# Kernel optimization log

Measured on AMD Instinct MI355X. Metric: run time of the kernel, lower is better.

## Reference

```python
import jax, jax.numpy as jnp
import numpy as np

N = 100000
E = 6400000
IN_CH = 128
HID = 8
HEADS = 2
OUT_CH = 1
NEG_SLOPE = 0.2


def gat_conv(x, src, dst, W, a_src, a_dst, bias, heads, out_ch, concat, n_nodes):
    # x: [N, F_in], W: [F_in, heads*out_ch], a_src/a_dst: [heads, out_ch]
    h = (x @ W).reshape(n_nodes, heads, out_ch)          # [N, H, C]
    alpha_s = jnp.sum(h * a_src[None], axis=-1)          # [N, H]
    alpha_d = jnp.sum(h * a_dst[None], axis=-1)          # [N, H]
    alpha = alpha_s[src] + alpha_d[dst]                  # [E, H]
    alpha = jax.nn.leaky_relu(alpha, NEG_SLOPE)
    # segment softmax over incoming edges of each destination node
    seg_max = jax.ops.segment_max(alpha, dst, num_segments=n_nodes)  # [N, H]
    alpha = jnp.exp(alpha - seg_max[dst])
    denom = jax.ops.segment_sum(alpha, dst, num_segments=n_nodes)    # [N, H]
    alpha = alpha / (denom[dst] + 1e-16)
    msg = h[src] * alpha[..., None]                       # [E, H, C]
    out = jax.ops.segment_sum(msg, dst, num_segments=n_nodes)        # [N, H, C]
    if concat:
        out = out.reshape(n_nodes, heads * out_ch)
    else:
        out = out.mean(axis=1)
    return out + bias


def setup_inputs() -> dict:
    key = jax.random.key(0)
    ks = jax.random.split(key, 12)
    x = jax.random.normal(ks[0], (N, IN_CH), dtype=jnp.float32)
    edge_index = jax.random.randint(ks[1], (2, E), 0, N, dtype=jnp.int64)
    s1 = 1.0 / np.sqrt(IN_CH)
    W1 = jax.random.normal(ks[2], (IN_CH, HEADS * HID), dtype=jnp.float32) * s1
    a_src1 = jax.random.normal(ks[3], (HEADS, HID), dtype=jnp.float32) * (1.0 / np.sqrt(HID))
    a_dst1 = jax.random.normal(ks[4], (HEADS, HID), dtype=jnp.float32) * (1.0 / np.sqrt(HID))
    b1 = jnp.zeros((HEADS * HID,), dtype=jnp.float32)
    s2 = 1.0 / np.sqrt(HEADS * HID)
    W2 = jax.random.normal(ks[5], (HEADS * HID, OUT_CH), dtype=jnp.float32) * s2
    a_src2 = jax.random.normal(ks[6], (1, OUT_CH), dtype=jnp.float32)
    a_dst2 = jax.random.normal(ks[7], (1, OUT_CH), dtype=jnp.float32)
    b2 = jnp.zeros((OUT_CH,), dtype=jnp.float32)
    return {"x": x, "edge_index": edge_index, "W1": W1, "a_src1": a_src1,
            "a_dst1": a_dst1, "b1": b1, "W2": W2, "a_src2": a_src2,
            "a_dst2": a_dst2, "b2": b2}


def reference(x, edge_index, W1, a_src1, a_dst1, b1, W2, a_src2, a_dst2, b2):
    # add self-loops (PyG GATConv default)
    loops = jnp.arange(N, dtype=edge_index.dtype)
    src = jnp.concatenate([edge_index[0], loops])
    dst = jnp.concatenate([edge_index[1], loops])
    h = gat_conv(x, src, dst, W1, a_src1, a_dst1, b1, HEADS, HID, True, N)
    h = jax.nn.relu(h)
    out = gat_conv(h, src, dst, W2, a_src2, a_dst2, b2, 1, OUT_CH, False, N)
    return out
```

## Files before the change

kernel.cpp:

```cpp
#include <hip/hip_runtime.h>
#include <hip/hip_fp16.h>
#include <cstdint>
#include <cstddef>

#define N_NODES 100000
#define E_EDGES 6400000
#define E_TOT   (E_EDGES + N_NODES)
#define IN_CH   128
#define NHID    16
#define BSHIFT  8
#define BSZ     256
#define NBUCK   391
#define CHUNK   8192
#define BCAP    24
#define NCHUNK  ((E_TOT + CHUNK - 1) / CHUNK)
#define LCAP    17664

__global__ void k_detect(const int* __restrict__ edge, int* __restrict__ flag) {
    if (blockIdx.x == 0 && threadIdx.x == 0) {
        int odd_or = 0;
        for (int i = 0; i < 64; i++) odd_or |= edge[2 * i + 1];
        flag[0] = (odd_or == 0) ? 1 : 0;
    }
}

__global__ __launch_bounds__(256) void k_gemm1(
        const float* __restrict__ x, const float* __restrict__ W1,
        const float* __restrict__ a_src1, const float* __restrict__ a_dst1,
        __half* __restrict__ h16, float* __restrict__ asrc,
        float* __restrict__ adst) {
    __shared__ __align__(16) float sW[IN_CH * NHID];
    __shared__ __align__(16) float sx[16][132];
    __shared__ float sh[16][17];
    int t = threadIdx.x;
    int r = t >> 4, c = t & 15;
    int row = blockIdx.x * 16 + r;

    const float4* W4 = (const float4*)W1;
    ((float4*)sW)[t] = W4[t];
    ((float4*)sW)[t + 256] = W4[t + 256];

    if (row < N_NODES) {
        const float4* xr = (const float4*)(x + (size_t)row * IN_CH);
        float4 v0 = xr[c];
        float4 v1 = xr[c + 16];
        *(float4*)&sx[r][4 * c] = v0;
        *(float4*)&sx[r][64 + 4 * c] = v1;
    }
    __syncthreads();

    float acc = 0.f;
    if (row < N_NODES) {
        #pragma unroll 16
        for (int k = 0; k < IN_CH; k++) acc = fmaf(sx[r][k], sW[k * NHID + c], acc);
        h16[(size_t)row * NHID + c] = __float2half(acc);
    }
    sh[r][c] = acc;
    __syncthreads();

    if (row < N_NODES && c < 4) {
        int h = c & 1;
        const float* av = (c >= 2) ? a_dst1 : a_src1;
        float s = 0.f;
        #pragma unroll
        for (int q = 0; q < 8; q++) s = fmaf(sh[r][h * 8 + q], av[h * 8 + q], s);
        if (c < 2) asrc[2 * (size_t)row + c] = s;
        else       adst[2 * (size_t)row + (c - 2)] = s;
    }
}

__global__ __launch_bounds__(256) void k_ccount(const int* __restrict__ edge,
                                                const int* __restrict__ flag,
                                                int* __restrict__ ccnt) {
    __shared__ int sc[NBUCK];
    int m64 = flag[0];
    int t = threadIdx.x;
    for (int i = t; i < NBUCK; i += 256) sc[i] = 0;
    __syncthreads();
    size_t c0 = (size_t)blockIdx.x * CHUNK;
    size_t cend = c0 + CHUNK; if (cend > E_TOT) cend = E_TOT;
    size_t ee = (cend < (size_t)E_EDGES) ? cend : (size_t)E_EDGES;

    if (m64) {
        const int4* dp = (const int4*)(edge + 2 * (size_t)E_EDGES);
        for (size_t i = c0 + 2 * t; i < ee; i += 512) {
            int4 v = dp[i >> 1];
            atomicAdd(&sc[v.x >> BSHIFT], 1);
            if (i + 1 < ee) atomicAdd(&sc[v.z >> BSHIFT], 1);
        }
    } else {
        const int4* dp = (const int4*)(edge + (size_t)E_EDGES);
        for (size_t i = c0 + 4 * t; i < ee; i += 1024) {
            int4 v = dp[i >> 2];
            atomicAdd(&sc[v.x >> BSHIFT], 1);
            if (i + 1 < ee) atomicAdd(&sc[v.y >> BSHIFT], 1);
            if (i + 2 < ee) atomicAdd(&sc[v.z >> BSHIFT], 1);
            if (i + 3 < ee) atomicAdd(&sc[v.w >> BSHIFT], 1);
        }
    }
    size_t sl0 = (c0 > (size_t)E_EDGES) ? c0 : (size_t)E_EDGES;
    for (size_t i = sl0 + t; i < cend; i += 256) {
        int d = (int)(i - E_EDGES);
        atomicAdd(&sc[d >> BSHIFT], 1);
    }
    __syncthreads();
    for (int i = t; i < NBUCK; i += 256)
        ccnt[(size_t)blockIdx.x * NBUCK + i] = sc[i];
}

__global__ __launch_bounds__(256) void k_cscan(int* __restrict__ ccnt,
                                               int* __restrict__ bcnt) {
    __shared__ int sd[256];
    __shared__ int carry;
    int b = blockIdx.x, t = threadIdx.x;
    if (t == 0) carry = 0;
    __syncthreads();
    for (int base = 0; base < NCHUNK; base += 256) {
        int c = base + t;
        int v = (c < NCHUNK) ? ccnt[(size_t)c * NBUCK + b] : 0;
        sd[t] = v;
        __syncthreads();
        for (int ofs = 1; ofs < 256; ofs <<= 1) {
            int a = sd[t];
            int bb = (t >= ofs) ? sd[t - ofs] : 0;
            __syncthreads();
            sd[t] = a + bb;
            __syncthreads();
        }
        if (c < NCHUNK) ccnt[(size_t)c * NBUCK + b] = sd[t] - v + carry;
        __syncthreads();
        if (t == 255) carry += sd[255];
        __syncthreads();
    }
    if (t == 0) bcnt[b] = carry;
}

__global__ __launch_bounds__(512) void k_bscan(const int* __restrict__ bcnt,
                                               int* __restrict__ bbase) {
    __shared__ int sd[512];
    int t = threadIdx.x;
    int v = (t < NBUCK) ? bcnt[t] : 0;
    sd[t] = v;
    __syncthreads();
    for (int ofs = 1; ofs < 512; ofs <<= 1) {
        int a = sd[t];
        int b = (t >= ofs) ? sd[t - ofs] : 0;
        __syncthreads();
        sd[t] = a + b;
        __syncthreads();
    }
    if (t < NBUCK) bbase[t] = sd[t] - v;
    if (t == NBUCK) bbase[NBUCK] = sd[NBUCK - 1];
}

__global__ __launch_bounds__(256) void k_bin(const int* __restrict__ edge,
                                             const int* __restrict__ flag,
                                             const int* __restrict__ ccnt,
                                             const int* __restrict__ bbase,
                                             unsigned* __restrict__ staged) {
    __shared__ unsigned lbin[NBUCK][BCAP];
    __shared__ int lcnt[NBUCK];
    __shared__ int lbase[NBUCK];
    int m64 = flag[0];
    int t = threadIdx.x;
    int g = t >> 4, lane = t & 15;

    size_t c0 = (size_t)blockIdx.x * CHUNK;
    if (c0 >= E_TOT) return;
    size_t cend = c0 + CHUNK; if (cend > E_TOT) cend = E_TOT;
    size_t ee = (cend < (size_t)E_EDGES) ? cend : (size_t)E_EDGES;

    for (int i = t; i < NBUCK; i += 256) {
        lcnt[i] = 0;
        lbase[i] = bbase[i] + ccnt[(size_t)blockIdx.x * NBUCK + i];
    }
    __syncthreads();

    auto put = [&](int s, int d) {
        int b = d >> BSHIFT;
        unsigned v = (unsigned)s | ((unsigned)(d & (BSZ - 1)) << 17);
        int idx = atomicAdd(&lcnt[b], 1);
        if (idx < BCAP) lbin[b][idx] = v;
        else            staged[lbase[b] + idx] = v;
    };

    if (m64) {
        const int4* sp = (const int4*)edge;
        const int4* dp = (const int4*)(edge + 2 * (size_t)E_EDGES);
        for (size_t i = c0 + 2 * t; i < ee; i += 512) {
            int4 sv = sp[i >> 1];
            int4 dv = dp[i >> 1];
            put(sv.x, dv.x);
            if (i + 1 < ee) put(sv.z, dv.z);
        }
    } else {
        const int4* sp = (const int4*)edge;
        const int4* dp = (const int4*)(edge + (size_t)E_EDGES);
        for (size_t i = c0 + 4 * t; i < ee; i += 1024) {
            int4 sv = sp[i >> 2];
            int4 dv = dp[i >> 2];
            put(sv.x, dv.x);
            if (i + 1 < ee) put(sv.y, dv.y);
            if (i + 2 < ee) put(sv.z, dv.z);
            if (i + 3 < ee) put(sv.w, dv.w);
        }
    }
    size_t sl0 = (c0 > (size_t)E_EDGES) ? c0 : (size_t)E_EDGES;
    for (size_t i = sl0 + t; i < cend; i += 256) {
        int d = (int)(i - E_EDGES);
        put(d, d);
    }
    __syncthreads();
    for (int b = g; b < NBUCK; b += 16) {
        int n = min(lcnt[b], BCAP);
        if (!n) continue;
        int pos = lbase[b];
        for (int i = lane; i < n; i += 16) staged[pos + i] = lbin[b][i];
    }
}

__global__ __launch_bounds__(512) void k_fused1(
        const unsigned* __restrict__ staged, const int* __restrict__ bbase,
        const __half* __restrict__ h16, const float* __restrict__ asrc,
        const float* __restrict__ adst,
        const float* __restrict__ b1, const float* __restrict__ W2,
        int* __restrict__ csr, int* __restrict__ offs,
        float* __restrict__ h2out) {
    __shared__ unsigned short lcsr16[LCAP];
    __shared__ unsigned hib[LCAP / 32];
    __shared__ int hist[BSZ];
    __shared__ int segbeg[BSZ];
    __shared__ int cur[BSZ];
    __shared__ float2 sadp[BSZ];
    int bkt = blockIdx.x;
    int t = threadIdx.x;
    int dbase = bkt << BSHIFT;
    int beg = bbase[bkt], end = bbase[bkt + 1];

    if (t < BSZ) {
        hist[t] = 0;
        int d = dbase + t;
        sadp[t] = (d < N_NODES) ? ((const float2*)adst)[d] : make_float2(0.f, 0.f);
    }
    for (int i = t; i < LCAP / 32; i += 512) hib[i] = 0;
    __syncthreads();
    for (int e = beg + t; e < end; e += 512)
        atomicAdd(&hist[staged[e] >> 17], 1);
    __syncthreads();

    int myv = (t < BSZ) ? hist[t] : 0;
    __syncthreads();
    for (int ofs = 1; ofs < BSZ; ofs <<= 1) {
        int a = 0, b = 0;
        if (t < BSZ) { a = hist[t]; b = (t >= ofs) ? hist[t - ofs] : 0; }
        __syncthreads();
        if (t < BSZ) hist[t] = a + b;
        __syncthreads();
    }
    if (t < BSZ) {
        int excl = hist[t] - myv;
        segbeg[t] = excl;
        cur[t] = excl;
        int d = dbase + t;
        if (d < N_NODES) offs[d] = beg + excl;
    }
    if (bkt == NBUCK - 1 && t == 0) offs[N_NODES] = E_TOT;
    __syncthreads();

    for (int e = beg + t; e < end; e += 512) {
        unsigned v = staged[e];
        int s = (int)(v & 0x1FFFFu);
        int pos = atomicAdd(&cur[v >> 17], 1);
        lcsr16[pos] = (unsigned short)s;
        if (s >> 16) atomicOr(&hib[pos >> 5], 1u << (pos & 31));
    }
    __syncthreads();

    auto getsrc = [&](int i) {
        return (int)lcsr16[i] | (int)(((hib[i >> 5] >> (i & 31)) & 1u) << 16);
    };

    int n = end - beg;
    for (int i = t; i < n; i += 512) csr[beg + i] = getsrc(i);

    int p = t >> 1, sub = t & 1;
    int sb = segbeg[p], se = cur[p];
    float adpv = sub ? sadp[p].y : sadp[p].x;

    float acc[8];
    #pragma unroll
    for (int c = 0; c < 8; c++) acc[c] = 0.f;
    float den = 0.f;

    auto loadslot = [&](int i, float& aspv, float4& hv) {
        if (i < se) {
            int s = getsrc(i);
            hv = *(const float4*)(h16 + (size_t)s * NHID + sub * 8);
            aspv = asrc[2 * (size_t)s + sub];
        }
    };
    auto consume = [&](float aspv, const float4& hv) {
        float a = aspv + adpv; a = (a > 0.f) ? a : 0.2f * a;
        float pw = __expf(a);
        den += pw;
        const __half2* hh = (const __half2*)&hv;
        #pragma unroll
        for (int q = 0; q < 4; q++) {
            float2 f = __half22float2(hh[q]);
            acc[2 * q]     = fmaf(pw, f.x, acc[2 * q]);
            acc[2 * q + 1] = fmaf(pw, f.y, acc[2 * q + 1]);
        }
    };

    float aA = 0.f, aB = 0.f, aC = 0.f, aD = 0.f, aE = 0.f, aF = 0.f;
    float4 z4 = make_float4(0.f, 0.f, 0.f, 0.f);
    float4 hA = z4, hB = z4, hC = z4, hD = z4, hE = z4, hF = z4;

    int i = sb;
    loadslot(i,     aA, hA);
    loadslot(i + 1, aB, hB);
    loadslot(i + 2, aC, hC);
    loadslot(i + 3, aD, hD);
    loadslot(i + 4, aE, hE);
    loadslot(i + 5, aF, hF);
    while (true) {
        if (i >= se) break;
        consume(aA, hA); loadslot(i + 6, aA, hA); i++;
        if (i >= se) break;
        consume(aB, hB); loadslot(i + 6, aB, hB); i++;
        if (i >= se) break;
        consume(aC, hC); loadslot(i + 6, aC, hC); i++;
        if (i >= se) break;
        consume(aD, hD); loadslot(i + 6, aD, hD); i++;
        if (i >= se) break;
        consume(aE, hE); loadslot(i + 6, aE, hE); i++;
        if (i >= se) break;
        consume(aF, hF); loadslot(i + 6, aF, hF); i++;
    }

    float inv = 1.f / (den + 1e-16f);
    float v = 0.f;
    #pragma unroll
    for (int ch = 0; ch < 8; ch++) {
        float o = acc[ch] * inv + b1[8 * sub + ch];
        o = (o > 0.f) ? o : 0.f;
        v = fmaf(o, W2[8 * sub + ch], v);
    }
    v += __shfl_xor(v, 1, 64);
    if (sub == 0) {
        int d = dbase + p;
        if (d < N_NODES) h2out[d] = v;
    }
}

__global__ __launch_bounds__(256) void k_edge2(
        const int* __restrict__ offs, const int* __restrict__ csr,
        const float* __restrict__ h2,
        const float* __restrict__ a_src2, const float* __restrict__ a_dst2,
        const float* __restrict__ b2, float* __restrict__ out) {
    int t = threadIdx.x;
    int g = t >> 4, lane = t & 15;
    int d = blockIdx.x * 16 + g;
    if (d >= N_NODES) return;

    float as2 = a_src2[0], ad2 = a_dst2[0];
    float adv = h2[d] * ad2;
    int beg = offs[d], end = offs[d + 1];

    float den = 0.f, acc = 0.f;
    auto ls = [&](int ee, float& hs) { if (ee < end) hs = h2[csr[ee]]; };
    auto cs = [&](float hs) {
        float a = fmaf(hs, as2, adv);
        a = (a > 0.f) ? a : 0.2f * a;
        float p = __expf(a);
        den += p;
        acc = fmaf(p, hs, acc);
    };
    float hA = 0.f, hB = 0.f, hC = 0.f, hD = 0.f, hE = 0.f, hF = 0.f;
    int e = beg + lane;
    ls(e, hA); ls(e + 16, hB); ls(e + 32, hC);
    ls(e + 48, hD); ls(e + 64, hE); ls(e + 80, hF);
    while (true) {
        if (e >= end) break;
        cs(hA); ls(e + 96, hA); e += 16;
        if (e >= end) break;
        cs(hB); ls(e + 96, hB); e += 16;
        if (e >= end) break;
        cs(hC); ls(e + 96, hC); e += 16;
        if (e >= end) break;
        cs(hD); ls(e + 96, hD); e += 16;
        if (e >= end) break;
        cs(hE); ls(e + 96, hE); e += 16;
        if (e >= end) break;
        cs(hF); ls(e + 96, hF); e += 16;
    }
    #pragma unroll
    for (int m = 1; m < 16; m <<= 1) {
        den += __shfl_xor(den, m, 64);
        acc += __shfl_xor(acc, m, 64);
    }
    if (lane == 0) out[d] = acc / (den + 1e-16f) + b2[0];
}

extern "C" void kernel_launch(void* const* d_in, const int* in_sizes, int n_in,
                              void* d_out, int out_size, void* d_ws, size_t ws_size,
                              hipStream_t stream) {
    const float* x      = (const float*)d_in[0];
    const int*   edge   = (const int*)  d_in[1];
    const float* W1     = (const float*)d_in[2];
    const float* a_src1 = (const float*)d_in[3];
    const float* a_dst1 = (const float*)d_in[4];
    const float* b1     = (const float*)d_in[5];
    const float* W2     = (const float*)d_in[6];
    const float* a_src2 = (const float*)d_in[7];
    const float* a_dst2 = (const float*)d_in[8];
    const float* b2     = (const float*)d_in[9];

    constexpr size_t A = 256;
    auto al = [](size_t b) { return (b + A - 1) / A * A; };
    char* ws = (char*)d_ws;
    size_t off = 0;
    int*      flag   = (int*)(ws + off);      off += al(256);
    int*      ccnt   = (int*)(ws + off);      off += al((size_t)NCHUNK * NBUCK * 4);
    int*      bcnt   = (int*)(ws + off);      off += al(NBUCK * 4);
    int*      bbase  = (int*)(ws + off);      off += al((NBUCK + 1) * 4);
    unsigned* staged = (unsigned*)(ws + off); off += al((size_t)E_TOT * 4);
    int*      csr    = (int*)(ws + off);      off += al((size_t)E_TOT * 4);
    int*      offs   = (int*)(ws + off);      off += al((size_t)(N_NODES + 1) * 4);
    __half*   h16    = (__half*)(ws + off);   off += al((size_t)N_NODES * NHID * 2);
    float*    asrc   = (float*)(ws + off);    off += al((size_t)N_NODES * 2 * 4);
    float*    adst   = (float*)(ws + off);    off += al((size_t)N_NODES * 2 * 4);
    float*    h2     = (float*)(ws + off);    off += al((size_t)N_NODES * 4);
    (void)ws_size; (void)in_sizes; (void)n_in; (void)out_size;

    k_detect<<<1, 64, 0, stream>>>(edge, flag);
    k_gemm1 <<<(N_NODES + 15) / 16, 256, 0, stream>>>(x, W1, a_src1, a_dst1, h16, asrc, adst);
    k_ccount<<<NCHUNK, 256, 0, stream>>>(edge, flag, ccnt);
    k_cscan <<<NBUCK, 256, 0, stream>>>(ccnt, bcnt);
    k_bscan <<<1, 512, 0, stream>>>(bcnt, bbase);
    k_bin   <<<NCHUNK, 256, 0, stream>>>(edge, flag, ccnt, bbase, staged);
    k_fused1<<<NBUCK, 512, 0, stream>>>(staged, bbase, h16, asrc, adst, b1, W2, csr, offs, h2);
    k_edge2 <<<(N_NODES + 15) / 16, 256, 0, stream>>>(offs, csr, h2, a_src2, a_dst2, b2,
                                                      (float*)d_out);
}
```

Baseline: 197.3 us.

## Replace count-scan-bin passes with fixed-size bucket slabs and atomic cursors

Removes the per-chunk counting pass and the two scan kernels. Each destination bucket now gets a fixed-capacity slab in the staging buffer, and binning claims slots with global atomic cursors padded to separate cache lines. Per-node end offsets are written separately so the CSR can have gaps between buckets. This saves a full read of the edge list and two dependent launches, at the cost of global atomics, a fixed slab capacity that relies on bucket sizes staying bounded for these inputs, and loss of the deterministic edge order.

```diff
diff --git a/kernel.cpp b/kernel.cpp
--- a/kernel.cpp
+++ b/kernel.cpp
@@ -12,9 +12,10 @@
 #define BSZ     256
 #define NBUCK   391
 #define CHUNK   8192
-#define BCAP    24
 #define NCHUNK  ((E_TOT + CHUNK - 1) / CHUNK)
+#define SLAB    17664
 #define LCAP    17664
+#define BCAP2   28
 
 __global__ void k_detect(const int* __restrict__ edge, int* __restrict__ flag) {
     if (blockIdx.x == 0 && threadIdx.x == 0) {
@@ -69,96 +70,16 @@
     }
 }
 
-__global__ __launch_bounds__(256) void k_ccount(const int* __restrict__ edge,
-                                                const int* __restrict__ flag,
-                                                int* __restrict__ ccnt) {
-    __shared__ int sc[NBUCK];
-    int m64 = flag[0];
-    int t = threadIdx.x;
-    for (int i = t; i < NBUCK; i += 256) sc[i] = 0;
-    __syncthreads();
-    size_t c0 = (size_t)blockIdx.x * CHUNK;
-    size_t cend = c0 + CHUNK; if (cend > E_TOT) cend = E_TOT;
-    size_t ee = (cend < (size_t)E_EDGES) ? cend : (size_t)E_EDGES;
-
-    if (m64) {
-        const int4* dp = (const int4*)(edge + 2 * (size_t)E_EDGES);
-        for (size_t i = c0 + 2 * t; i < ee; i += 512) {
-            int4 v = dp[i >> 1];
-            atomicAdd(&sc[v.x >> BSHIFT], 1);
-            if (i + 1 < ee) atomicAdd(&sc[v.z >> BSHIFT], 1);
-        }
-    } else {
-        const int4* dp = (const int4*)(edge + (size_t)E_EDGES);
-        for (size_t i = c0 + 4 * t; i < ee; i += 1024) {
-            int4 v = dp[i >> 2];
-            atomicAdd(&sc[v.x >> BSHIFT], 1);
-            if (i + 1 < ee) atomicAdd(&sc[v.y >> BSHIFT], 1);
-            if (i + 2 < ee) atomicAdd(&sc[v.z >> BSHIFT], 1);
-            if (i + 3 < ee) atomicAdd(&sc[v.w >> BSHIFT], 1);
-        }
-    }
-    size_t sl0 = (c0 > (size_t)E_EDGES) ? c0 : (size_t)E_EDGES;
-    for (size_t i = sl0 + t; i < cend; i += 256) {
-        int d = (int)(i - E_EDGES);
-        atomicAdd(&sc[d >> BSHIFT], 1);
-    }
-    __syncthreads();
-    for (int i = t; i < NBUCK; i += 256)
-        ccnt[(size_t)blockIdx.x * NBUCK + i] = sc[i];
-}
-
-__global__ __launch_bounds__(256) void k_cscan(int* __restrict__ ccnt,
-                                               int* __restrict__ bcnt) {
-    __shared__ int sd[256];
-    __shared__ int carry;
-    int b = blockIdx.x, t = threadIdx.x;
-    if (t == 0) carry = 0;
-    __syncthreads();
-    for (int base = 0; base < NCHUNK; base += 256) {
-        int c = base + t;
-        int v = (c < NCHUNK) ? ccnt[(size_t)c * NBUCK + b] : 0;
-        sd[t] = v;
-        __syncthreads();
-        for (int ofs = 1; ofs < 256; ofs <<= 1) {
-            int a = sd[t];
-            int bb = (t >= ofs) ? sd[t - ofs] : 0;
-            __syncthreads();
-            sd[t] = a + bb;
-            __syncthreads();
-        }
-        if (c < NCHUNK) ccnt[(size_t)c * NBUCK + b] = sd[t] - v + carry;
-        __syncthreads();
-        if (t == 255) carry += sd[255];
-        __syncthreads();
-    }
-    if (t == 0) bcnt[b] = carry;
-}
-
-__global__ __launch_bounds__(512) void k_bscan(const int* __restrict__ bcnt,
-                                               int* __restrict__ bbase) {
-    __shared__ int sd[512];
-    int t = threadIdx.x;
-    int v = (t < NBUCK) ? bcnt[t] : 0;
-    sd[t] = v;
-    __syncthreads();
-    for (int ofs = 1; ofs < 512; ofs <<= 1) {
-        int a = sd[t];
-        int b = (t >= ofs) ? sd[t - ofs] : 0;
-        __syncthreads();
-        sd[t] = a + b;
-        __syncthreads();
-    }
-    if (t < NBUCK) bbase[t] = sd[t] - v;
-    if (t == NBUCK) bbase[NBUCK] = sd[NBUCK - 1];
-}
-
-__global__ __launch_bounds__(256) void k_bin(const int* __restrict__ edge,
-                                             const int* __restrict__ flag,
-                                             const int* __restrict__ ccnt,
-                                             const int* __restrict__ bbase,
-                                             unsigned* __restrict__ staged) {
-    __shared__ unsigned lbin[NBUCK][BCAP];
+__global__ void k_binit(int* __restrict__ bcur) {
+    int i = blockIdx.x * 256 + threadIdx.x;
+    if (i < NBUCK) bcur[i * 16] = i * SLAB;
+}
+
+__global__ __launch_bounds__(256) void k_bin2(const int* __restrict__ edge,
+                                              const int* __restrict__ flag,
+                                              int* __restrict__ bcur,
+                                              unsigned* __restrict__ staged) {
+    __shared__ unsigned lbin[NBUCK][BCAP2];
     __shared__ int lcnt[NBUCK];
     __shared__ int lbase[NBUCK];
     int m64 = flag[0];
@@ -170,18 +91,18 @@
     size_t cend = c0 + CHUNK; if (cend > E_TOT) cend = E_TOT;
     size_t ee = (cend < (size_t)E_EDGES) ? cend : (size_t)E_EDGES;
 
-    for (int i = t; i < NBUCK; i += 256) {
-        lcnt[i] = 0;
-        lbase[i] = bbase[i] + ccnt[(size_t)blockIdx.x * NBUCK + i];
-    }
+    for (int i = t; i < NBUCK; i += 256) lcnt[i] = 0;
     __syncthreads();
 
     auto put = [&](int s, int d) {
         int b = d >> BSHIFT;
         unsigned v = (unsigned)s | ((unsigned)(d & (BSZ - 1)) << 17);
         int idx = atomicAdd(&lcnt[b], 1);
-        if (idx < BCAP) lbin[b][idx] = v;
-        else            staged[lbase[b] + idx] = v;
+        if (idx < BCAP2) lbin[b][idx] = v;
+        else {
+            int slot = atomicAdd(&bcur[b * 16], 1);
+            staged[slot] = v;
+        }
     };
 
     if (m64) {
@@ -211,8 +132,15 @@
         put(d, d);
     }
     __syncthreads();
+
+    for (int b = t; b < NBUCK; b += 256) {
+        int n = lcnt[b]; if (n > BCAP2) n = BCAP2;
+        if (n) lbase[b] = atomicAdd(&bcur[b * 16], n);
+    }
+    __syncthreads();
+
     for (int b = g; b < NBUCK; b += 16) {
-        int n = min(lcnt[b], BCAP);
+        int n = lcnt[b]; if (n > BCAP2) n = BCAP2;
         if (!n) continue;
         int pos = lbase[b];
         for (int i = lane; i < n; i += 16) staged[pos + i] = lbin[b][i];
@@ -220,11 +148,11 @@
 }
 
 __global__ __launch_bounds__(512) void k_fused1(
-        const unsigned* __restrict__ staged, const int* __restrict__ bbase,
+        const unsigned* __restrict__ staged, const int* __restrict__ bcur,
         const __half* __restrict__ h16, const float* __restrict__ asrc,
         const float* __restrict__ adst,
         const float* __restrict__ b1, const float* __restrict__ W2,
-        int* __restrict__ csr, int* __restrict__ offs,
+        int* __restrict__ csr, int* __restrict__ offs, int* __restrict__ eoffs,
         float* __restrict__ h2out) {
     __shared__ unsigned short lcsr16[LCAP];
     __shared__ unsigned hib[LCAP / 32];
@@ -235,7 +163,8 @@
     int bkt = blockIdx.x;
     int t = threadIdx.x;
     int dbase = bkt << BSHIFT;
-    int beg = bbase[bkt], end = bbase[bkt + 1];
+    int beg = bkt * SLAB;
+    int end = bcur[bkt * 16];
 
     if (t < BSZ) {
         hist[t] = 0;
@@ -264,7 +193,6 @@
         int d = dbase + t;
         if (d < N_NODES) offs[d] = beg + excl;
     }
-    if (bkt == NBUCK - 1 && t == 0) offs[N_NODES] = E_TOT;
     __syncthreads();
 
     for (int e = beg + t; e < end; e += 512) {
@@ -275,6 +203,11 @@
         if (s >> 16) atomicOr(&hib[pos >> 5], 1u << (pos & 31));
     }
     __syncthreads();
+
+    if (t < BSZ) {
+        int d = dbase + t;
+        if (d < N_NODES) eoffs[d] = beg + cur[t];
+    }
 
     auto getsrc = [&](int i) {
         return (int)lcsr16[i] | (int)(((hib[i >> 5] >> (i & 31)) & 1u) << 16);
@@ -354,8 +287,8 @@
 }
 
 __global__ __launch_bounds__(256) void k_edge2(
-        const int* __restrict__ offs, const int* __restrict__ csr,
-        const float* __restrict__ h2,
+        const int* __restrict__ offs, const int* __restrict__ eoffs,
+        const int* __restrict__ csr, const float* __restrict__ h2,
         const float* __restrict__ a_src2, const float* __restrict__ a_dst2,
         const float* __restrict__ b2, float* __restrict__ out) {
     int t = threadIdx.x;
@@ -365,7 +298,7 @@
 
     float as2 = a_src2[0], ad2 = a_dst2[0];
     float adv = h2[d] * ad2;
-    int beg = offs[d], end = offs[d + 1];
+    int beg = offs[d], end = eoffs[d];
 
     float den = 0.f, acc = 0.f;
     auto ls = [&](int ee, float& hs) { if (ee < end) hs = h2[csr[ee]]; };
@@ -421,12 +354,11 @@
     char* ws = (char*)d_ws;
     size_t off = 0;
     int*      flag   = (int*)(ws + off);      off += al(256);
-    int*      ccnt   = (int*)(ws + off);      off += al((size_t)NCHUNK * NBUCK * 4);
-    int*      bcnt   = (int*)(ws + off);      off += al(NBUCK * 4);
-    int*      bbase  = (int*)(ws + off);      off += al((NBUCK + 1) * 4);
-    unsigned* staged = (unsigned*)(ws + off); off += al((size_t)E_TOT * 4);
-    int*      csr    = (int*)(ws + off);      off += al((size_t)E_TOT * 4);
-    int*      offs   = (int*)(ws + off);      off += al((size_t)(N_NODES + 1) * 4);
+    int*      bcur   = (int*)(ws + off);      off += al((size_t)NBUCK * 16 * 4);
+    unsigned* staged = (unsigned*)(ws + off); off += al((size_t)NBUCK * SLAB * 4);
+    int*      csr    = (int*)(ws + off);      off += al((size_t)NBUCK * SLAB * 4);
+    int*      offs   = (int*)(ws + off);      off += al((size_t)N_NODES * 4);
+    int*      eoffs  = (int*)(ws + off);      off += al((size_t)N_NODES * 4);
     __half*   h16    = (__half*)(ws + off);   off += al((size_t)N_NODES * NHID * 2);
     float*    asrc   = (float*)(ws + off);    off += al((size_t)N_NODES * 2 * 4);
     float*    adst   = (float*)(ws + off);    off += al((size_t)N_NODES * 2 * 4);
@@ -435,11 +367,10 @@
 
     k_detect<<<1, 64, 0, stream>>>(edge, flag);
     k_gemm1 <<<(N_NODES + 15) / 16, 256, 0, stream>>>(x, W1, a_src1, a_dst1, h16, asrc, adst);
-    k_ccount<<<NCHUNK, 256, 0, stream>>>(edge, flag, ccnt);
-    k_cscan <<<NBUCK, 256, 0, stream>>>(ccnt, bcnt);
-    k_bscan <<<1, 512, 0, stream>>>(bcnt, bbase);
-    k_bin   <<<NCHUNK, 256, 0, stream>>>(edge, flag, ccnt, bbase, staged);
-    k_fused1<<<NBUCK, 512, 0, stream>>>(staged, bbase, h16, asrc, adst, b1, W2, csr, offs, h2);
-    k_edge2 <<<(N_NODES + 15) / 16, 256, 0, stream>>>(offs, csr, h2, a_src2, a_dst2, b2,
-                                                      (float*)d_out);
-}
+    k_binit <<<2, 256, 0, stream>>>(bcur);
+    k_bin2  <<<NCHUNK, 256, 0, stream>>>(edge, flag, bcur, staged);
+    k_fused1<<<NBUCK, 512, 0, stream>>>(staged, bcur, h16, asrc, adst, b1, W2,
+                                        csr, offs, eoffs, h2);
+    k_edge2 <<<(N_NODES + 15) / 16, 256, 0, stream>>>(offs, eoffs, csr, h2,
+                                                      a_src2, a_dst2, b2, (float*)d_out);
+}
```

Measured after the change: 305.4 us. 1.55x slower.
